# Performance work log

Measured on AMD Instinct MI355X. Metric: run time of the kernel, lower is better.

## Reference

```python
import jax, jax.numpy as jnp
import numpy as np

N_EMBED = 2048
N_HEAD = 16
HEAD_DIM = N_EMBED // N_HEAD  # 128


def setup_inputs() -> dict:
    key = jax.random.key(0)
    k1, k2, k3 = jax.random.split(key, 3)
    B, S = 2, 2048
    x = jax.random.normal(k1, (B, S, N_EMBED), dtype=jnp.float32)
    # torch Linear weight [out,in]; store transposed for x @ W
    scale_attn = 1.0 / np.sqrt(N_EMBED)
    w_attn = jax.random.normal(k2, (N_EMBED, (N_HEAD + 2) * HEAD_DIM), dtype=jnp.float32) * scale_attn
    w_out = jax.random.normal(k3, (N_EMBED, N_EMBED), dtype=jnp.float32) * scale_attn
    return {"x": x, "w_attn": w_attn, "w_out": w_out}


def reference(x, w_attn, w_out):
    B, S, E = x.shape
    H, D = N_HEAD, HEAD_DIM
    qkv = x @ w_attn                               # [B,S,(H+2)*D]
    q, k, v = jnp.split(qkv, [E, E + D], axis=2)   # [B,S,E], [B,S,D], [B,S,D]
    q = q.reshape(B, S, H, D).transpose(0, 2, 1, 3)  # [B,H,S,D]
    # single shared K/V head (MQA)
    scores = jnp.einsum("bhsd,btd->bhst", q, k) * (D ** -0.5)  # [B,H,S,S]
    p = jax.nn.softmax(scores, axis=-1)
    attn = jnp.einsum("bhst,btd->bhsd", p, v)      # [B,H,S,D]
    attn = attn.transpose(0, 2, 1, 3).reshape(B, S, E)
    return attn @ w_out
```

## Files before the change

kernel.cpp:

```cpp
#include <hip/hip_runtime.h>
#include <hip/hip_bf16.h>

typedef __attribute__((ext_vector_type(8))) short short8;
typedef __attribute__((ext_vector_type(4))) float f32x4;

#define GLOBAL_AS __attribute__((address_space(1)))
#define LDS_AS    __attribute__((address_space(3)))

__device__ __forceinline__ unsigned short f2bf(float f) {
    union { float f; unsigned int u; } v; v.f = f;
    unsigned int r = v.u + 0x7FFFu + ((v.u >> 16) & 1u);
    return (unsigned short)(r >> 16);
}

__device__ __forceinline__ unsigned int pk_bf16(float a, float b) {
    union { __hip_bfloat162 h; unsigned int u; } c;
    c.h = __float22bfloat162_rn(float2{a, b});
    return c.u;
}

__device__ __forceinline__ short8 cvt8v(float4 a, float4 b) {
    union { short8 s; unsigned int u[4]; } c;
    c.u[0] = pk_bf16(a.x, a.y); c.u[1] = pk_bf16(a.z, a.w);
    c.u[2] = pk_bf16(b.x, b.y); c.u[3] = pk_bf16(b.z, b.w);
    return c.s;
}

__device__ __forceinline__ void async_ld16(const unsigned short* g, unsigned short* l) {
    __builtin_amdgcn_global_load_lds((const GLOBAL_AS unsigned int*)g,
                                     (LDS_AS unsigned int*)l, 16, 0, 0);
}

__global__ __launch_bounds__(256) void cvt_bf16(
    const float* __restrict__ src, unsigned short* __restrict__ dst)
{
    const size_t i = ((size_t)blockIdx.x * 256 + threadIdx.x) * 8;
    float4 a = *(const float4*)(src + i);
    float4 b = *(const float4*)(src + i + 4);
    *(short8*)(dst + i) = cvt8v(a, b);
}

__global__ __launch_bounds__(256) void transpose_cvt(
    const float* __restrict__ src, unsigned short* __restrict__ dst, int K, int N)
{
    __shared__ unsigned short t[64][72];
    const int tid = threadIdx.x;
    const int n0 = blockIdx.x * 64, k0 = blockIdx.y * 64;
    #pragma unroll
    for (int it = 0; it < 4; ++it) {
        int r = it * 16 + (tid >> 4);
        int c = (tid & 15) * 4;
        float4 v = *(const float4*)(src + (size_t)(k0 + r) * N + n0 + c);
        t[r][c] = f2bf(v.x); t[r][c + 1] = f2bf(v.y);
        t[r][c + 2] = f2bf(v.z); t[r][c + 3] = f2bf(v.w);
    }
    __syncthreads();
    const int nr = tid >> 2, kg = (tid & 3) * 16;
    short8 o0, o1;
    #pragma unroll
    for (int j = 0; j < 8; ++j) { o0[j] = (short)t[kg + j][nr]; o1[j] = (short)t[kg + 8 + j][nr]; }
    *(short8*)(dst + (size_t)(n0 + nr) * K + k0 + kg) = o0;
    *(short8*)(dst + (size_t)(n0 + nr) * K + k0 + kg + 8) = o1;
}

template<bool OUT_F32>
__global__ __launch_bounds__(256, 2) void gemm_bt(
    const unsigned short* __restrict__ Ab, const unsigned short* __restrict__ Bt,
    void* __restrict__ Cv, int M, int N, int K)
{
    __shared__ __align__(16) unsigned short As[2][128][64];
    __shared__ __align__(16) unsigned short Bs[2][128][64];

    const int tid = threadIdx.x, lane = tid & 63, w = tid >> 6;
    const int quad = lane >> 4, l15 = lane & 15;

    const int nwg = gridDim.x * gridDim.y;
    int lin = blockIdx.y * gridDim.x + blockIdx.x;
    lin = (lin & 7) * (nwg >> 3) + (lin >> 3);
    const int m0 = (lin / gridDim.x) * 128, n0 = (lin % gridDim.x) * 128;

    const int rw = (w >> 1) * 64, cw = (w & 1) * 64;

    const f32x4 zero = {0.f, 0.f, 0.f, 0.f};
    f32x4 acc[4][4];
    #pragma unroll
    for (int i = 0; i < 4; ++i)
        #pragma unroll
        for (int j = 0; j < 4; ++j) acc[i][j] = zero;

    const int srow = lane >> 3;
    const int scol = ((lane & 7) ^ srow) * 8;
    const int rx = (l15 & 7) << 3;

    #pragma unroll
    for (int c = 0; c < 4; ++c) {
        async_ld16(Ab + (size_t)(m0 + w * 32 + c * 8 + srow) * K + scol,
                   &As[0][w * 32 + c * 8][0]);
        async_ld16(Bt + (size_t)(n0 + w * 32 + c * 8 + srow) * K + scol,
                   &Bs[0][w * 32 + c * 8][0]);
    }

    int p = 0;
    for (int k0 = 0; k0 < K; k0 += 64) {
        __syncthreads();

        if (k0 + 64 < K) {
            #pragma unroll
            for (int c = 0; c < 4; ++c) {
                async_ld16(Ab + (size_t)(m0 + w * 32 + c * 8 + srow) * K + k0 + 64 + scol,
                           &As[p ^ 1][w * 32 + c * 8][0]);
                async_ld16(Bt + (size_t)(n0 + w * 32 + c * 8 + srow) * K + k0 + 64 + scol,
                           &Bs[p ^ 1][w * 32 + c * 8][0]);
            }
        }

        const unsigned short* Asf = &As[p][0][0];
        const unsigned short* Bsf = &Bs[p][0][0];
        short8 af[4][2], bf2[4][2];
        #pragma unroll
        for (int i = 0; i < 4; ++i) {
            const int rb = (rw + i * 16 + l15) * 64;
            af[i][0] = *(const short8*)(Asf + ((rb + quad * 8) ^ rx));
            af[i][1] = *(const short8*)(Asf + ((rb + 32 + quad * 8) ^ rx));
        }
        #pragma unroll
        for (int j = 0; j < 4; ++j) {
            const int rb = (cw + j * 16 + l15) * 64;
            bf2[j][0] = *(const short8*)(Bsf + ((rb + quad * 8) ^ rx));
            bf2[j][1] = *(const short8*)(Bsf + ((rb + 32 + quad * 8) ^ rx));
        }

        #pragma unroll
        for (int i = 0; i < 4; ++i)
            #pragma unroll
            for (int j = 0; j < 4; ++j) {
                acc[i][j] = __builtin_amdgcn_mfma_f32_16x16x32_bf16(af[i][0], bf2[j][0], acc[i][j], 0, 0, 0);
                acc[i][j] = __builtin_amdgcn_mfma_f32_16x16x32_bf16(af[i][1], bf2[j][1], acc[i][j], 0, 0, 0);
            }

        p ^= 1;
    }

    #pragma unroll
    for (int i = 0; i < 4; ++i) {
        const int row = m0 + rw + i * 16 + quad * 4;
        #pragma unroll
        for (int j = 0; j < 4; ++j) {
            const int col = n0 + cw + j * 16 + l15;
            #pragma unroll
            for (int r = 0; r < 4; ++r) {
                if constexpr (OUT_F32)
                    ((float*)Cv)[(size_t)(row + r) * N + col] = acc[i][j][r];
                else
                    ((unsigned short*)Cv)[(size_t)(row + r) * N + col] = f2bf(acc[i][j][r]);
            }
        }
    }
}

__global__ __launch_bounds__(256) void mqa_flash(
    const unsigned short* __restrict__ qkv,
    unsigned short* __restrict__ attn)
{
    const int S = 2048, QKVW = 2304;
    __shared__ __align__(16) union {
        struct {
            unsigned short Ks[2][32][136];
            unsigned short VT[2][144][44];
        } s;
        unsigned short T[4][32][136];
    } sm;

    const int tid = threadIdx.x, lane = tid & 63, w = tid >> 6;
    const int quad = lane >> 4, l15 = lane & 15;
    const int bid = blockIdx.x;
    const int qb = bid & 15;
    const int h  = (bid >> 4) & 15;
    const int b  = bid >> 8;

    for (int i = tid; i < 2 * 16 * 32; i += 256)
        sm.s.VT[i >> 9][128 + ((i >> 5) & 15)][i & 31] = 0x3F80;

    const unsigned short* base = qkv + (size_t)b * S * QKVW;

    short8 qf[2][4];
    #pragma unroll
    for (int sub = 0; sub < 2; ++sub) {
        const int row = qb * 128 + w * 32 + sub * 16 + l15;
        #pragma unroll
        for (int ds = 0; ds < 4; ++ds)
            qf[sub][ds] = *(const short8*)(base + (size_t)row * QKVW + h * 128 + ds * 32 + quad * 8);
    }

    const f32x4 zero = {0.f, 0.f, 0.f, 0.f};
    f32x4 o[2][9];
    #pragma unroll
    for (int sub = 0; sub < 2; ++sub)
        #pragma unroll
        for (int d = 0; d < 9; ++d) o[sub][d] = zero;

    const int krow = tid & 31, kdg = tid >> 5;
    const int kpr  = ((krow & 1) << 4) | (krow >> 1);
    const int vkp  = tid & 15, vdg = tid >> 4;

    const unsigned short* kp = base + (size_t)krow * QKVW + 2048 + kdg * 16;
    const unsigned short* vp = base + (size_t)(2 * vkp) * QKVW + 2176 + vdg * 8;

    short8 k0v = *(const short8*)kp;
    short8 k1v = *(const short8*)(kp + 8);
    short8 v0v = *(const short8*)vp;
    short8 v1v = *(const short8*)(vp + QKVW);

    for (int kb = 0; kb < S; kb += 32) {
        const int p = (kb >> 5) & 1;

        *(short8*)(&sm.s.Ks[p][kpr][kdg * 16]) = k0v;
        *(short8*)(&sm.s.Ks[p][kpr][kdg * 16 + 8]) = k1v;
        #pragma unroll
        for (int j = 0; j < 8; ++j) {
            unsigned int pkv = (unsigned int)(unsigned short)v0v[j]
                             | ((unsigned int)(unsigned short)v1v[j] << 16);
            *(unsigned int*)(&sm.s.VT[p][vdg * 8 + j][vkp * 2]) = pkv;
        }

        if (kb + 32 < S) {
            kp += 32 * QKVW; vp += 32 * QKVW;
            k0v = *(const short8*)kp;
            k1v = *(const short8*)(kp + 8);
            v0v = *(const short8*)vp;
            v1v = *(const short8*)(vp + QKVW);
        }

        __syncthreads();

        __builtin_amdgcn_s_setprio(1);

        f32x4 sc[2][2];
        sc[0][0] = zero; sc[0][1] = zero; sc[1][0] = zero; sc[1][1] = zero;
        #pragma unroll
        for (int ds = 0; ds < 4; ++ds) {
            short8 kf0 = *(const short8*)(&sm.s.Ks[p][l15][ds * 32 + quad * 8]);
            short8 kf1 = *(const short8*)(&sm.s.Ks[p][16 + l15][ds * 32 + quad * 8]);
            #pragma unroll
            for (int sub = 0; sub < 2; ++sub) {
                sc[sub][0] = __builtin_amdgcn_mfma_f32_16x16x32_bf16(kf0, qf[sub][ds], sc[sub][0], 0, 0, 0);
                sc[sub][1] = __builtin_amdgcn_mfma_f32_16x16x32_bf16(kf1, qf[sub][ds], sc[sub][1], 0, 0, 0);
            }
        }

        const float scale = 0.08838834764831845f;
        short8 pf[2];
        #pragma unroll
        for (int sub = 0; sub < 2; ++sub) {
            union { short8 sv; unsigned int u[4]; } c;
            #pragma unroll
            for (int r = 0; r < 4; ++r) {
                float e0 = __expf(fmaf(sc[sub][0][r], scale, -12.f));
                float e1 = __expf(fmaf(sc[sub][1][r], scale, -12.f));
                c.u[r] = pk_bf16(e0, e1);
            }
            pf[sub] = c.sv;
        }

        #pragma unroll
        for (int dsub = 0; dsub < 9; ++dsub) {
            short8 vf = *(const short8*)(&sm.s.VT[p][dsub * 16 + l15][quad * 8]);
            o[0][dsub] = __builtin_amdgcn_mfma_f32_16x16x32_bf16(vf, pf[0], o[0][dsub], 0, 0, 0);
            o[1][dsub] = __builtin_amdgcn_mfma_f32_16x16x32_bf16(vf, pf[1], o[1][dsub], 0, 0, 0);
        }

        __builtin_amdgcn_s_setprio(0);
    }

    __syncthreads();

    #pragma unroll
    for (int sub = 0; sub < 2; ++sub) {
        const float inv = 1.0f / o[sub][8][0];
        #pragma unroll
        for (int dsub = 0; dsub < 8; ++dsub) {
            unsigned int lo = pk_bf16(o[sub][dsub][0] * inv, o[sub][dsub][1] * inv);
            unsigned int hi = pk_bf16(o[sub][dsub][2] * inv, o[sub][dsub][3] * inv);
            unsigned int* dst = (unsigned int*)&sm.T[w][sub * 16 + l15][dsub * 16 + quad * 4];
            dst[0] = lo; dst[1] = hi;
        }
    }
    __syncthreads();

    const size_t rowbase = (size_t)b * S + qb * 128 + w * 32;
    #pragma unroll
    for (int pass = 0; pass < 8; ++pass) {
        const int row = pass * 4 + quad;
        short8 ov = *(const short8*)(&sm.T[w][row][l15 * 8]);
        *(short8*)(&attn[(rowbase + row) * 2048 + h * 128 + l15 * 8]) = ov;
    }
}

extern "C" void kernel_launch(void* const* d_in, const int* in_sizes, int n_in,
                              void* d_out, int out_size, void* d_ws, size_t ws_size,
                              hipStream_t stream)
{
    const float* x     = (const float*)d_in[0];
    const float* wattn = (const float*)d_in[1];
    const float* wout  = (const float*)d_in[2];
    float* out = (float*)d_out;

    unsigned short* ws = (unsigned short*)d_ws;
    unsigned short* qkv    = ws;
    unsigned short* woutT  = ws;
    unsigned short* wattnT = ws + (size_t)9437184;
    unsigned short* attn   = ws + (size_t)9437184;
    unsigned short* xb     = (unsigned short*)d_out;

    cvt_bf16<<<dim3(4096), 256, 0, stream>>>(x, xb);
    transpose_cvt<<<dim3(2304 / 64, 2048 / 64), 256, 0, stream>>>(wattn, wattnT, 2048, 2304);
    gemm_bt<false><<<dim3(2304 / 128, 4096 / 128), 256, 0, stream>>>(
        xb, wattnT, qkv, 4096, 2304, 2048);
    mqa_flash<<<dim3(2 * 16 * 16), 256, 0, stream>>>(qkv, attn);
    transpose_cvt<<<dim3(2048 / 64, 2048 / 64), 256, 0, stream>>>(wout, woutT, 2048, 2048);
    gemm_bt<true><<<dim3(2048 / 128, 4096 / 128), 256, 0, stream>>>(
        attn, woutT, out, 4096, 2048, 2048);
}
```

Measured before the change: 295.1 us.

## Rework GEMM mainloop into 4-stage K=32 pipeline with explicit vmcnt waits

Replaces the double-buffered K=64 LDS pipeline in the bf16 GEMM with four K=32 stage buffers, keeping three tiles in flight. Each step waits with an explicit s_waitcnt vmcnt and a raw barrier instead of __syncthreads. The swizzle changes to a 4-chunk XOR pattern to suit the narrower rows. The aim is to hide more global-load latency and reduce barrier stalls, at the cost of more barriers per K and a fixed remainder structure that assumes K is a multiple of 128 and at least 256.

```diff
diff --git a/kernel.cpp b/kernel.cpp
--- a/kernel.cpp
+++ b/kernel.cpp
@@ -30,6 +30,9 @@
     __builtin_amdgcn_global_load_lds((const GLOBAL_AS unsigned int*)g,
                                      (LDS_AS unsigned int*)l, 16, 0, 0);
 }
+
+#define WAITV(N) asm volatile("s_waitcnt vmcnt(" #N ")" ::: "memory")
+#define BARSYNC() do { __builtin_amdgcn_s_barrier(); __builtin_amdgcn_sched_barrier(0); } while (0)
 
 __global__ __launch_bounds__(256) void cvt_bf16(
     const float* __restrict__ src, unsigned short* __restrict__ dst)
@@ -63,13 +66,47 @@
     *(short8*)(dst + (size_t)(n0 + nr) * K + k0 + kg + 8) = o1;
 }
 
+__device__ __forceinline__ void stage_tile(
+    const unsigned short* __restrict__ Ag, const unsigned short* __restrict__ Bg,
+    unsigned short (*Asb)[32], unsigned short (*Bsb)[32],
+    int m0, int n0, int K, int k, int w, int srow, int scol)
+{
+    #pragma unroll
+    for (int c = 0; c < 2; ++c) {
+        const int rb = c * 64 + w * 16;
+        async_ld16(Ag + (size_t)(m0 + rb + srow) * K + k + scol, &Asb[rb][0]);
+        async_ld16(Bg + (size_t)(n0 + rb + srow) * K + k + scol, &Bsb[rb][0]);
+    }
+}
+
+__device__ __forceinline__ void compute_tile(
+    const unsigned short (*Asb)[32], const unsigned short (*Bsb)[32],
+    int rw, int cw, int l15, int quad, f32x4 acc[4][4])
+{
+    const int pc = (quad ^ (l15 & 3)) * 8;
+    short8 af[4], bf[4];
+    #pragma unroll
+    for (int i = 0; i < 4; ++i)
+        af[i] = *(const short8*)&Asb[rw + i * 16 + l15][pc];
+    #pragma unroll
+    for (int j = 0; j < 4; ++j)
+        bf[j] = *(const short8*)&Bsb[cw + j * 16 + l15][pc];
+    #pragma unroll
+    for (int i = 0; i < 4; ++i)
+        #pragma unroll
+        for (int j = 0; j < 4; ++j)
+            acc[i][j] = __builtin_amdgcn_mfma_f32_16x16x32_bf16(af[i], bf[j], acc[i][j], 0, 0, 0);
+}
+
 template<bool OUT_F32>
 __global__ __launch_bounds__(256, 2) void gemm_bt(
     const unsigned short* __restrict__ Ab, const unsigned short* __restrict__ Bt,
     void* __restrict__ Cv, int M, int N, int K)
 {
-    __shared__ __align__(16) unsigned short As[2][128][64];
-    __shared__ __align__(16) unsigned short Bs[2][128][64];
+    __shared__ __align__(16) unsigned short As0[128][32], Bs0[128][32];
+    __shared__ __align__(16) unsigned short As1[128][32], Bs1[128][32];
+    __shared__ __align__(16) unsigned short As2[128][32], Bs2[128][32];
+    __shared__ __align__(16) unsigned short As3[128][32], Bs3[128][32];
 
     const int tid = threadIdx.x, lane = tid & 63, w = tid >> 6;
     const int quad = lane >> 4, l15 = lane & 15;
@@ -88,57 +125,45 @@
         #pragma unroll
         for (int j = 0; j < 4; ++j) acc[i][j] = zero;
 
-    const int srow = lane >> 3;
-    const int scol = ((lane & 7) ^ srow) * 8;
-    const int rx = (l15 & 7) << 3;
-
-    #pragma unroll
-    for (int c = 0; c < 4; ++c) {
-        async_ld16(Ab + (size_t)(m0 + w * 32 + c * 8 + srow) * K + scol,
-                   &As[0][w * 32 + c * 8][0]);
-        async_ld16(Bt + (size_t)(n0 + w * 32 + c * 8 + srow) * K + scol,
-                   &Bs[0][w * 32 + c * 8][0]);
-    }
-
-    int p = 0;
-    for (int k0 = 0; k0 < K; k0 += 64) {
-        __syncthreads();
-
-        if (k0 + 64 < K) {
-            #pragma unroll
-            for (int c = 0; c < 4; ++c) {
-                async_ld16(Ab + (size_t)(m0 + w * 32 + c * 8 + srow) * K + k0 + 64 + scol,
-                           &As[p ^ 1][w * 32 + c * 8][0]);
-                async_ld16(Bt + (size_t)(n0 + w * 32 + c * 8 + srow) * K + k0 + 64 + scol,
-                           &Bs[p ^ 1][w * 32 + c * 8][0]);
-            }
-        }
-
-        const unsigned short* Asf = &As[p][0][0];
-        const unsigned short* Bsf = &Bs[p][0][0];
-        short8 af[4][2], bf2[4][2];
-        #pragma unroll
-        for (int i = 0; i < 4; ++i) {
-            const int rb = (rw + i * 16 + l15) * 64;
-            af[i][0] = *(const short8*)(Asf + ((rb + quad * 8) ^ rx));
-            af[i][1] = *(const short8*)(Asf + ((rb + 32 + quad * 8) ^ rx));
-        }
-        #pragma unroll
-        for (int j = 0; j < 4; ++j) {
-            const int rb = (cw + j * 16 + l15) * 64;
-            bf2[j][0] = *(const short8*)(Bsf + ((rb + quad * 8) ^ rx));
-            bf2[j][1] = *(const short8*)(Bsf + ((rb + 32 + quad * 8) ^ rx));
-        }
-
-        #pragma unroll
-        for (int i = 0; i < 4; ++i)
-            #pragma unroll
-            for (int j = 0; j < 4; ++j) {
-                acc[i][j] = __builtin_amdgcn_mfma_f32_16x16x32_bf16(af[i][0], bf2[j][0], acc[i][j], 0, 0, 0);
-                acc[i][j] = __builtin_amdgcn_mfma_f32_16x16x32_bf16(af[i][1], bf2[j][1], acc[i][j], 0, 0, 0);
-            }
-
-        p ^= 1;
+    const int srow = lane >> 2;
+    const int scol = (((lane & 3) ^ (srow & 3)) * 8);
+
+    stage_tile(Ab, Bt, As0, Bs0, m0, n0, K, 0,  w, srow, scol);
+    stage_tile(Ab, Bt, As1, Bs1, m0, n0, K, 32, w, srow, scol);
+    stage_tile(Ab, Bt, As2, Bs2, m0, n0, K, 64, w, srow, scol);
+
+    for (int k0 = 0; k0 + 224 < K; k0 += 128) {
+        WAITV(8); BARSYNC();
+        stage_tile(Ab, Bt, As3, Bs3, m0, n0, K, k0 + 96, w, srow, scol);
+        compute_tile(As0, Bs0, rw, cw, l15, quad, acc);
+
+        WAITV(8); BARSYNC();
+        stage_tile(Ab, Bt, As0, Bs0, m0, n0, K, k0 + 128, w, srow, scol);
+        compute_tile(As1, Bs1, rw, cw, l15, quad, acc);
+
+        WAITV(8); BARSYNC();
+        stage_tile(Ab, Bt, As1, Bs1, m0, n0, K, k0 + 160, w, srow, scol);
+        compute_tile(As2, Bs2, rw, cw, l15, quad, acc);
+
+        WAITV(8); BARSYNC();
+        stage_tile(Ab, Bt, As2, Bs2, m0, n0, K, k0 + 192, w, srow, scol);
+        compute_tile(As3, Bs3, rw, cw, l15, quad, acc);
+    }
+
+    {
+        const int kt = K - 128;
+        WAITV(8); BARSYNC();
+        stage_tile(Ab, Bt, As3, Bs3, m0, n0, K, kt + 96, w, srow, scol);
+        compute_tile(As0, Bs0, rw, cw, l15, quad, acc);
+
+        WAITV(8); BARSYNC();
+        compute_tile(As1, Bs1, rw, cw, l15, quad, acc);
+
+        WAITV(4); BARSYNC();
+        compute_tile(As2, Bs2, rw, cw, l15, quad, acc);
+
+        WAITV(0); BARSYNC();
+        compute_tile(As3, Bs3, rw, cw, l15, quad, acc);
     }
 
     #pragma unroll
```

Measured after the change: 289.5 us. About the same (-1.9%).
